# Kernel optimization log

Measured on AMD Instinct MI355X. Metric: run time of the kernel, lower is better.

Reference implementation:

```python
import jax, jax.numpy as jnp
import numpy as np

G = 4  # number of groups


def _group_vals(h, shift, Ua, Ua1, Ua2, Ua3):
    # h: [B, H]; Ua: [g, H/g, r]; Ua1/2/3: [g, r, H/g]
    B, H = h.shape
    hg = h.reshape(B, G, H // G)
    if shift:
        # torch index = rotate-left by `shift`: new group j reads old group (j+shift)%g
        hg = jnp.roll(hg, -shift, axis=1)
    t = jnp.einsum('bgd,gdr->bgr', hg, Ua)  # shared low-rank projection
    proj = lambda M: jnp.einsum('bgr,grd->bgd', t, M).reshape(B, H)
    return proj(Ua1), proj(Ua2), proj(Ua3)


def setup_inputs() -> dict:
    key = jax.random.key(0)
    ks = jax.random.split(key, 24)
    B, I, H, wR = 8192, 1024, 1024, 256
    hg = H // G
    r01, r23 = 64, 32
    d = {}
    d['x'] = jax.random.normal(ks[0], (B, I), dtype=jnp.float32)
    d['h'] = jax.random.normal(ks[1], (B, H), dtype=jnp.float32)
    d['W'] = 0.1 * jax.random.normal(ks[2], (I, wR), dtype=jnp.float32)
    d['W1'] = 0.1 * jax.random.normal(ks[3], (wR, H), dtype=jnp.float32)
    d['W2'] = 0.1 * jax.random.normal(ks[4], (wR, H), dtype=jnp.float32)
    d['W3'] = 0.1 * jax.random.normal(ks[5], (wR, H), dtype=jnp.float32)
    d['U'] = 0.1 * jax.random.normal(ks[6], (G, hg, r01), dtype=jnp.float32)
    d['U1'] = 0.1 * jax.random.normal(ks[7], (G, r01, hg), dtype=jnp.float32)
    d['U2'] = 0.1 * jax.random.normal(ks[8], (G, r01, hg), dtype=jnp.float32)
    d['U3'] = 0.1 * jax.random.normal(ks[9], (G, r01, hg), dtype=jnp.float32)
    d['UU'] = 0.1 * jax.random.normal(ks[10], (G, hg, r01), dtype=jnp.float32)
    d['UU1'] = 0.1 * jax.random.normal(ks[11], (G, r01, hg), dtype=jnp.float32)
    d['UU2'] = 0.1 * jax.random.normal(ks[12], (G, r01, hg), dtype=jnp.float32)
    d['UU3'] = 0.1 * jax.random.normal(ks[13], (G, r01, hg), dtype=jnp.float32)
    d['UUU'] = 0.1 * jax.random.normal(ks[14], (G, hg, r23), dtype=jnp.float32)
    d['UUU1'] = 0.1 * jax.random.normal(ks[15], (G, r23, hg), dtype=jnp.float32)
    d['UUU2'] = 0.1 * jax.random.normal(ks[16], (G, r23, hg), dtype=jnp.float32)
    d['UUU3'] = 0.1 * jax.random.normal(ks[17], (G, r23, hg), dtype=jnp.float32)
    d['UUUU'] = 0.1 * jax.random.normal(ks[18], (G, hg, r23), dtype=jnp.float32)
    d['UUUU1'] = 0.1 * jax.random.normal(ks[19], (G, r23, hg), dtype=jnp.float32)
    d['UUUU2'] = 0.1 * jax.random.normal(ks[20], (G, r23, hg), dtype=jnp.float32)
    d['UUUU3'] = 0.1 * jax.random.normal(ks[21], (G, r23, hg), dtype=jnp.float32)
    d['bias_r'] = jnp.ones((1, H), dtype=jnp.float32)
    d['bias_gate'] = jnp.ones((1, H), dtype=jnp.float32)
    d['bias_update'] = jnp.ones((1, H), dtype=jnp.float32)
    return d


def reference(x, h, W, W1, W2, W3, U, U1, U2, U3, UU, UU1, UU2, UU3,
              UUU, UUU1, UUU2, UUU3, UUUU, UUUU1, UUUU2, UUUU3,
              bias_r, bias_gate, bias_update):
    u1, u2, u3 = _group_vals(h, 0, U, U1, U2, U3)
    uu1, uu2, uu3 = _group_vals(h, 1, UU, UU1, UU2, UU3)
    uuu1, uuu2, uuu3 = _group_vals(h, 2, UUU, UUU1, UUU2, UUU3)
    uuuu1, uuuu2, uuuu3 = _group_vals(h, 3, UUUU, UUUU1, UUUU2, UUUU3)
    xw = x @ W  # [B, wRank]
    w1, w2, w3 = xw @ W1, xw @ W2, xw @ W3
    r = jax.nn.sigmoid(w1 + u1 + uu1 + uuu1 + uuuu1 + bias_r)
    z = jax.nn.sigmoid(w2 + u2 + uu2 + uuu2 + uuuu2 + bias_gate)
    c_tilda = jnp.tanh(w3 + r * (u3 + uu3 + uuu3 + uuuu3) + bias_update)
    return z * h + (1.0 - z) * c_tilda
```

## Files before the change

kernel.cpp:

```cpp
#include <hip/hip_runtime.h>

typedef short bf16x8 __attribute__((ext_vector_type(8)));
typedef float f32x4 __attribute__((ext_vector_type(4)));
typedef float f32x16 __attribute__((ext_vector_type(16)));

__device__ __forceinline__ unsigned short f2bf(float f) {
  union { float f; unsigned u; } c; c.f = f;
  unsigned u = c.u;
  u += 0x7FFFu + ((u >> 16) & 1u);
  return (unsigned short)(u >> 16);
}
__device__ __forceinline__ float bf2f(unsigned short h) {
  union { unsigned u; float f; } c; c.u = ((unsigned)h) << 16;
  return c.f;
}
__device__ __forceinline__ void split2(float v, unsigned short& hi, unsigned short& lo) {
  union { float f; unsigned u; } c; c.f = v;
  unsigned uh = c.u & 0xFFFF0000u;
  hi = (unsigned short)(uh >> 16);
  union { unsigned u; float f; } d; d.u = uh;
  lo = f2bf(v - d.f);
}
__device__ __forceinline__ void gload16(const void* g, void* l) {
  __builtin_amdgcn_global_load_lds((const __attribute__((address_space(1))) void*)g,
                                   (__attribute__((address_space(3))) void*)l, 16, 0, 0);
}
__device__ __forceinline__ float sigm(float x) { return 1.0f / (1.0f + __expf(-x)); }
__device__ __forceinline__ float tanha(float x) { return 1.0f - 2.0f / (1.0f + __expf(2.0f * x)); }

__device__ __forceinline__ size_t fragIdxA(int row, int col) {
  int mb = row >> 7, rb = (row >> 5) & 3, l5 = row & 31;
  int cc = col >> 6, k4 = (col >> 4) & 3, hi = (col >> 3) & 1, e = col & 7;
  return ((size_t)(mb * 20 + cc) * 16 + rb * 4 + k4) * 512 + (hi * 32 + l5) * 8 + e;
}

__global__ __launch_bounds__(256) void s123(
    const float* __restrict__ W,
    const float* __restrict__ U, const float* __restrict__ UU,
    const float* __restrict__ UUU, const float* __restrict__ UUUU,
    const float* __restrict__ W1, const float* __restrict__ W2, const float* __restrict__ W3,
    const float* __restrict__ A1, const float* __restrict__ A2, const float* __restrict__ A3,
    const float* __restrict__ B1, const float* __restrict__ B2, const float* __restrict__ B3,
    const float* __restrict__ C1, const float* __restrict__ C2, const float* __restrict__ C3,
    const float* __restrict__ D1, const float* __restrict__ D2, const float* __restrict__ D3,
    unsigned short* __restrict__ Wt, unsigned short* __restrict__ Bg,
    unsigned short* __restrict__ Btp) {
  int gidx = blockIdx.x * 256 + threadIdx.x;
  if (gidx < 262144) {
    int idx = gidx;
    int n = idx >> 10, k = idx & 1023;
    Wt[idx] = f2bf(W[k * 256 + n]);
  } else if (gidx < 458752) {
    int idx = gidx - 262144;
    int g = idx / 49152;
    int rem = idx - g * 49152;
    int n = rem >> 8, k = rem & 255;
    int jj = 0, rr = n;
#pragma unroll
    for (int s = 0; s < 3; ++s) {
      int w = (((g - jj) & 3) < 2) ? 64 : 32;
      if (rr >= w) { rr -= w; ++jj; }
    }
    int v = (g - jj) & 3;
    int rv = (v < 2) ? 64 : 32;
    const float* M = (v == 0) ? U : (v == 1) ? UU : (v == 2) ? UUU : UUUU;
    Bg[idx] = f2bf(M[(jj * 256 + k) * rv + rr]);
  } else {
    int idx = gidx - 458752;
    int blk = idx / 12288;
    int w   = idx - blk * 12288;
    int frag = w >> 9, fl = (w >> 3) & 63, e = w & 7;
    int cb = blk & 3, jk = blk >> 2;
    int kt = jk % 11, j = jk / 11;
    int q = frag >> 3, colblk = (frag >> 2) & 1, k4 = frag & 3;
    int c  = cb * 64 + colblk * 32 + (fl & 31);
    int k2 = k4 * 16 + (fl >> 5) * 8 + e;
    float val;
    if (kt < 8) {
      int kk = (kt * 64 + k2) & 255;
      const float* Wp = (q == 0) ? W1 : (q == 1) ? W2 : W3;
      val = Wp[kk * 1024 + j * 256 + c];
    } else {
      int kT = (kt - 8) * 64 + k2;
      int v, r, rv;
      if (kT < 64)       { v = 0; r = kT;       rv = 64; }
      else if (kT < 128) { v = 1; r = kT - 64;  rv = 64; }
      else if (kT < 160) { v = 2; r = kT - 128; rv = 32; }
      else               { v = 3; r = kT - 160; rv = 32; }
      const float* M;
      if (v == 0)      M = (q == 0) ? A1 : (q == 1) ? A2 : A3;
      else if (v == 1) M = (q == 0) ? B1 : (q == 1) ? B2 : B3;
      else if (v == 2) M = (q == 0) ? C1 : (q == 1) ? C2 : C3;
      else             M = (q == 0) ? D1 : (q == 1) ? D2 : D3;
      val = M[(j * rv + r) * 256 + c];
    }
    Btp[idx] = f2bf(val);
  }
}

__global__ __launch_bounds__(256) void g1_xw(const float* __restrict__ x,
                                             const unsigned short* __restrict__ Wt,
                                             unsigned short* __restrict__ Abuf) {
  __shared__ char lds[49152];
  const int tid = threadIdx.x, lane = tid & 63, wid = tid >> 6;
  const int mb = blockIdx.x, nb = blockIdx.y;
  const int wn = wid;
  f32x4 acc[2][2] = {};
  float4 xr[2];
  const int r0 = tid >> 4, f4c = tid & 15;
  const float* xbase = x + (size_t)(mb * 32) * 1024 + f4c * 4;

  auto loadX = [&](int kt) {
#pragma unroll
    for (int q = 0; q < 2; ++q)
      xr[q] = *(const float4*)(xbase + (size_t)(q * 16 + r0) * 1024 + kt * 64);
  };
  auto writeA = [&](int buf) {
#pragma unroll
    for (int q = 0; q < 2; ++q) {
      int row = q * 16 + r0;
      float4 v = xr[q];
      unsigned short h0, h1, h2, h3, l0, l1, l2, l3;
      split2(v.x, h0, l0); split2(v.y, h1, l1);
      split2(v.z, h2, l2); split2(v.w, h3, l3);
      int ba = row * 128 + ((f4c * 8) ^ ((row & 7) << 4));
      *(uint2*)(lds + buf * 4096 + ba) =
          make_uint2(((unsigned)h1 << 16) | h0, ((unsigned)h3 << 16) | h2);
      *(uint2*)(lds + 8192 + buf * 4096 + ba) =
          make_uint2(((unsigned)l1 << 16) | l0, ((unsigned)l3 << 16) | l2);
    }
  };
  auto stageB = [&](int kt, int buf) {
#pragma unroll
    for (int it = 0; it < 4; ++it) {
      int nloc = it * 32 + wid * 8 + (lane >> 3);
      const char* src = (const char*)Wt + (size_t)(nb * 128 + nloc) * 2048 + kt * 128
                        + (((lane & 7) * 16) ^ ((nloc & 7) << 4));
      gload16(src, lds + 16384 + buf * 16384 + (it * 32 + wid * 8) * 128);
    }
  };

  loadX(0); stageB(0, 0); writeA(0);
  __syncthreads();
#pragma unroll 2
  for (int kt = 0; kt < 16; ++kt) {
    int buf = kt & 1;
    if (kt < 15) {
      loadX(kt + 1); stageB(kt + 1, buf ^ 1);
      asm volatile("s_waitcnt vmcnt(6)" ::: "memory");
    } else {
      asm volatile("s_waitcnt vmcnt(0)" ::: "memory");
    }
    __builtin_amdgcn_s_barrier();
    __builtin_amdgcn_sched_barrier(0);
    const char* hA = lds + buf * 4096;
    const char* lA = lds + 8192 + buf * 4096;
    const char* bB = lds + 16384 + buf * 16384;
#pragma unroll
    for (int ks = 0; ks < 2; ++ks) {
      bf16x8 ah[2], al[2], b[2];
#pragma unroll
      for (int mf = 0; mf < 2; ++mf) {
        int mloc = mf * 16 + (lane & 15);
        int ka = (ks * 64 + (lane >> 4) * 16) ^ ((mloc & 7) << 4);
        ah[mf] = *(const bf16x8*)(hA + mloc * 128 + ka);
        al[mf] = *(const bf16x8*)(lA + mloc * 128 + ka);
      }
#pragma unroll
      for (int nf = 0; nf < 2; ++nf) {
        int nloc = wn * 32 + nf * 16 + (lane & 15);
        int kb = (ks * 64 + (lane >> 4) * 16) ^ ((nloc & 7) << 4);
        b[nf] = *(const bf16x8*)(bB + nloc * 128 + kb);
      }
#pragma unroll
      for (int mf = 0; mf < 2; ++mf)
#pragma unroll
        for (int nf = 0; nf < 2; ++nf) {
          acc[mf][nf] = __builtin_amdgcn_mfma_f32_16x16x32_bf16(ah[mf], b[nf], acc[mf][nf], 0, 0, 0);
          acc[mf][nf] = __builtin_amdgcn_mfma_f32_16x16x32_bf16(al[mf], b[nf], acc[mf][nf], 0, 0, 0);
        }
    }
    if (kt < 15) writeA(buf ^ 1);
    __builtin_amdgcn_sched_barrier(0);
    asm volatile("s_waitcnt lgkmcnt(0)" ::: "memory");
    __builtin_amdgcn_s_barrier();
  }
#pragma unroll
  for (int mf = 0; mf < 2; ++mf)
#pragma unroll
    for (int nf = 0; nf < 2; ++nf)
#pragma unroll
      for (int r = 0; r < 4; ++r) {
        int row = mb * 32 + mf * 16 + (lane >> 4) * 4 + r;
        int col = nb * 128 + wn * 32 + nf * 16 + (lane & 15);
        float val = acc[mf][nf][r];
        unsigned short hi, lo;
        split2(val, hi, lo);
        Abuf[fragIdxA(row, col)] = hi;
        Abuf[fragIdxA(row, col + 256)] = lo;
      }
}

__global__ __launch_bounds__(256) void g2_t(const float* __restrict__ h,
                                            const unsigned short* __restrict__ Bg,
                                            unsigned short* __restrict__ Abuf) {
  __shared__ char lds[65536];
  const int tid = threadIdx.x, lane = tid & 63, wid = tid >> 6;
  const int mb = blockIdx.x, g = blockIdx.y;
  const int wm = wid >> 1, wn = wid & 1;
  f32x4 acc[2][6] = {};
  float4 hr[4];
  const int r0 = tid >> 4, f4c = tid & 15;
  const float* hbase = h + (size_t)(mb * 64) * 1024 + g * 256 + f4c * 4;

  auto loadH = [&](int kt) {
#pragma unroll
    for (int q = 0; q < 4; ++q)
      hr[q] = *(const float4*)(hbase + (size_t)(q * 16 + r0) * 1024 + kt * 64);
  };
  auto writeA = [&](int buf) {
#pragma unroll
    for (int q = 0; q < 4; ++q) {
      int row = q * 16 + r0;
      float4 v = hr[q];
      int ba = row * 128 + ((f4c * 8) ^ ((row & 7) << 4));
      *(uint2*)(lds + buf * 8192 + ba) =
          make_uint2(((unsigned)f2bf(v.y) << 16) | f2bf(v.x),
                     ((unsigned)f2bf(v.w) << 16) | f2bf(v.z));
    }
  };
  auto stageB = [&](int kt, int buf) {
#pragma unroll
    for (int it = 0; it < 6; ++it) {
      int nloc = it * 32 + wid * 8 + (lane >> 3);
      const char* src = (const char*)Bg + (size_t)(g * 192 + nloc) * 512 + kt * 128
                        + (((lane & 7) * 16) ^ ((nloc & 7) << 4));
      gload16(src, lds + 16384 + buf * 24576 + (it * 32 + wid * 8) * 128);
    }
  };

  loadH(0); stageB(0, 0); writeA(0);
  __syncthreads();
#pragma unroll
  for (int kt = 0; kt < 4; ++kt) {
    int buf = kt & 1;
    if (kt < 3) { loadH(kt + 1); stageB(kt + 1, buf ^ 1); }
    const char* cA = lds + buf * 8192;
    const char* cB = lds + 16384 + buf * 24576;
#pragma unroll
    for (int ks = 0; ks < 2; ++ks) {
      bf16x8 a[2], b[6];
#pragma unroll
      for (int mf = 0; mf < 2; ++mf) {
        int mloc = wm * 32 + mf * 16 + (lane & 15);
        int ka = (ks * 64 + (lane >> 4) * 16) ^ ((mloc & 7) << 4);
        a[mf] = *(const bf16x8*)(cA + mloc * 128 + ka);
      }
#pragma unroll
      for (int nf = 0; nf < 6; ++nf) {
        int nloc = wn * 96 + nf * 16 + (lane & 15);
        int kb = (ks * 64 + (lane >> 4) * 16) ^ ((nloc & 7) << 4);
        b[nf] = *(const bf16x8*)(cB + nloc * 128 + kb);
      }
#pragma unroll
      for (int mf = 0; mf < 2; ++mf)
#pragma unroll
        for (int nf = 0; nf < 6; ++nf)
          acc[mf][nf] = __builtin_amdgcn_mfma_f32_16x16x32_bf16(a[mf], b[nf], acc[mf][nf], 0, 0, 0);
    }
    if (kt < 3) writeA(buf ^ 1);
    __syncthreads();
  }
#pragma unroll
  for (int mf = 0; mf < 2; ++mf)
#pragma unroll
    for (int nf = 0; nf < 6; ++nf) {
      int n = wn * 96 + nf * 16 + (lane & 15);
      int jj = 0, rr = n;
#pragma unroll
      for (int s = 0; s < 3; ++s) {
        int w = (((g - jj) & 3) < 2) ? 64 : 32;
        if (rr >= w) { rr -= w; ++jj; }
      }
      int v = (g - jj) & 3;
      int offv = (v < 2) ? (v << 6) : (64 + (v << 5));
      int col = 512 + jj * 192 + offv + rr;
#pragma unroll
      for (int r = 0; r < 4; ++r) {
        int row = mb * 64 + wm * 32 + mf * 16 + (lane >> 4) * 4 + r;
        Abuf[fragIdxA(row, col)] = f2bf(acc[mf][nf][r]);
      }
    }
}

__global__ __launch_bounds__(256) void g3_main(const unsigned short* __restrict__ Abuf,
                                               const unsigned short* __restrict__ Btp,
                                               const float* __restrict__ h,
                                               const float* __restrict__ bias_r,
                                               const float* __restrict__ bias_g,
                                               const float* __restrict__ bias_u,
                                               float* __restrict__ out) {
  __shared__ char lds[81920];
  const int tid = threadIdx.x, lane = tid & 63, wid = tid >> 6;
  const int mb = blockIdx.x, cb = blockIdx.y, j = blockIdx.z;
  const int wm = wid >> 1, wn = wid & 1;
  f32x16 acc[2][4] = {};

  const char* AbufB = (const char*)Abuf;
  const char* BtpB  = (const char*)Btp;

  auto stage = [&](int kt, int buf) {
    int cc = (kt < 8) ? kt : (8 + j * 3 + (kt - 8));
    const char* asrc = AbufB + (size_t)(mb * 20 + cc) * 16384 + tid * 16;
    const char* bsrc = BtpB + (size_t)(((j * 11 + kt) * 4 + cb)) * 24576 + tid * 16;
#pragma unroll
    for (int it = 0; it < 4; ++it)
      gload16(asrc + it * 4096, lds + buf * 16384 + it * 4096 + wid * 1024);
#pragma unroll
    for (int it = 0; it < 6; ++it)
      gload16(bsrc + it * 4096, lds + 32768 + buf * 24576 + it * 4096 + wid * 1024);
  };

  stage(0, 0);
#pragma unroll
  for (int kt = 0; kt < 11; ++kt) {
    const int buf = kt & 1;
    if (kt < 10) {
      stage(kt + 1, buf ^ 1);
      asm volatile("s_waitcnt vmcnt(10)" ::: "memory");
    } else {
      asm volatile("s_waitcnt vmcnt(0)" ::: "memory");
    }
    __builtin_amdgcn_s_barrier();
    __builtin_amdgcn_sched_barrier(0);
    __builtin_amdgcn_s_setprio(1);
    const char* aB = lds + buf * 16384 + wm * 8192 + lane * 16;
    const char* bB = lds + 32768 + buf * 24576 + wn * 4096 + lane * 16;
#pragma unroll
    for (int k4 = 0; k4 < 4; ++k4) {
      bf16x8 a0 = *(const bf16x8*)(aB + k4 * 1024);
      bf16x8 a1 = *(const bf16x8*)(aB + 4096 + k4 * 1024);
#pragma unroll
      for (int q = 0; q < 3; ++q) {
        const int p = (kt < 8) ? q : ((q == 2) ? 3 : q);
        bf16x8 b = *(const bf16x8*)(bB + q * 8192 + k4 * 1024);
        acc[0][p] = __builtin_amdgcn_mfma_f32_32x32x16_bf16(a0, b, acc[0][p], 0, 0, 0);
        acc[1][p] = __builtin_amdgcn_mfma_f32_32x32x16_bf16(a1, b, acc[1][p], 0, 0, 0);
      }
    }
    __builtin_amdgcn_s_setprio(0);
    __builtin_amdgcn_sched_barrier(0);
    __builtin_amdgcn_s_barrier();
  }
  int cg = j * 256 + cb * 64 + wn * 32 + (lane & 31);
  float br = bias_r[cg], bg = bias_g[cg], bu = bias_u[cg];
#pragma unroll
  for (int mblk = 0; mblk < 2; ++mblk)
#pragma unroll
    for (int r = 0; r < 16; ++r) {
      int row = mb * 128 + wm * 64 + mblk * 32 + (r & 3) + 8 * (r >> 2) + 4 * (lane >> 5);
      float p0 = acc[mblk][0][r], p1 = acc[mblk][1][r];
      float p2 = acc[mblk][2][r], p3 = acc[mblk][3][r];
      float rr = sigm(p0 + br);
      float zz = sigm(p1 + bg);
      float ct = tanha(p2 + rr * p3 + bu);
      float hv = h[(size_t)row * 1024 + cg];
      out[(size_t)row * 1024 + cg] = zz * hv + (1.0f - zz) * ct;
    }
}

extern "C" void kernel_launch(void* const* d_in, const int* in_sizes, int n_in,
                              void* d_out, int out_size, void* d_ws, size_t ws_size,
                              hipStream_t stream) {
  const float* x   = (const float*)d_in[0];
  const float* h   = (const float*)d_in[1];
  const float* W   = (const float*)d_in[2];
  const float* W1  = (const float*)d_in[3];
  const float* W2  = (const float*)d_in[4];
  const float* W3  = (const float*)d_in[5];
  const float* U   = (const float*)d_in[6];
  const float* U1  = (const float*)d_in[7];
  const float* U2  = (const float*)d_in[8];
  const float* U3  = (const float*)d_in[9];
  const float* UU   = (const float*)d_in[10];
  const float* UU1  = (const float*)d_in[11];
  const float* UU2  = (const float*)d_in[12];
  const float* UU3  = (const float*)d_in[13];
  const float* UUU   = (const float*)d_in[14];
  const float* UUU1  = (const float*)d_in[15];
  const float* UUU2  = (const float*)d_in[16];
  const float* UUU3  = (const float*)d_in[17];
  const float* UUUU   = (const float*)d_in[18];
  const float* UUUU1  = (const float*)d_in[19];
  const float* UUUU2  = (const float*)d_in[20];
  const float* UUUU3  = (const float*)d_in[21];
  const float* bias_r = (const float*)d_in[22];
  const float* bias_g = (const float*)d_in[23];
  const float* bias_u = (const float*)d_in[24];

  char* ws = (char*)d_ws;
  unsigned short* Abuf = (unsigned short*)(ws);
  unsigned short* Wt   = (unsigned short*)(ws + 20971520);
  unsigned short* Bg   = (unsigned short*)(ws + 21495808);
  unsigned short* Btp  = (unsigned short*)(ws + 21889024);
  float* out = (float*)d_out;

  s123<<<10240, 256, 0, stream>>>(W, U, UU, UUU, UUUU,
                                  W1, W2, W3, U1, U2, U3, UU1, UU2, UU3,
                                  UUU1, UUU2, UUU3, UUUU1, UUUU2, UUUU3,
                                  Wt, Bg, Btp);
  g1_xw<<<dim3(256, 2), 256, 0, stream>>>(x, Wt, Abuf);
  g2_t<<<dim3(128, 4), 256, 0, stream>>>(h, Bg, Abuf);
  g3_main<<<dim3(64, 4, 4), 256, 0, stream>>>(Abuf, Btp, h, bias_r, bias_g, bias_u, out);
}
```

Baseline: 94.70 us.

## Widen g1 tile to full N and remap g3 blocks per XCD

```diff
diff --git a/kernel.cpp b/kernel.cpp
--- a/kernel.cpp
+++ b/kernel.cpp
@@ -101,11 +101,11 @@
 __global__ __launch_bounds__(256) void g1_xw(const float* __restrict__ x,
                                              const unsigned short* __restrict__ Wt,
                                              unsigned short* __restrict__ Abuf) {
-  __shared__ char lds[49152];
+  __shared__ char lds[81920];
   const int tid = threadIdx.x, lane = tid & 63, wid = tid >> 6;
-  const int mb = blockIdx.x, nb = blockIdx.y;
-  const int wn = wid;
-  f32x4 acc[2][2] = {};
+  const int mb = blockIdx.x;
+  const int wm = wid >> 1, wn = wid & 1;
+  f32x4 acc[8] = {};
   float4 xr[2];
   const int r0 = tid >> 4, f4c = tid & 15;
   const float* xbase = x + (size_t)(mb * 32) * 1024 + f4c * 4;
@@ -132,22 +132,21 @@
   };
   auto stageB = [&](int kt, int buf) {
 #pragma unroll
-    for (int it = 0; it < 4; ++it) {
+    for (int it = 0; it < 8; ++it) {
       int nloc = it * 32 + wid * 8 + (lane >> 3);
-      const char* src = (const char*)Wt + (size_t)(nb * 128 + nloc) * 2048 + kt * 128
+      const char* src = (const char*)Wt + (size_t)nloc * 2048 + kt * 128
                         + (((lane & 7) * 16) ^ ((nloc & 7) << 4));
-      gload16(src, lds + 16384 + buf * 16384 + (it * 32 + wid * 8) * 128);
+      gload16(src, lds + 16384 + buf * 32768 + (it * 32 + wid * 8) * 128);
     }
   };
 
   loadX(0); stageB(0, 0); writeA(0);
   __syncthreads();
-#pragma unroll 2
   for (int kt = 0; kt < 16; ++kt) {
     int buf = kt & 1;
     if (kt < 15) {
       loadX(kt + 1); stageB(kt + 1, buf ^ 1);
-      asm volatile("s_waitcnt vmcnt(6)" ::: "memory");
+      asm volatile("s_waitcnt vmcnt(10)" ::: "memory");
     } else {
       asm volatile("s_waitcnt vmcnt(0)" ::: "memory");
     }
@@ -155,30 +154,21 @@
     __builtin_amdgcn_sched_barrier(0);
     const char* hA = lds + buf * 4096;
     const char* lA = lds + 8192 + buf * 4096;
-    const char* bB = lds + 16384 + buf * 16384;
+    const char* bB = lds + 16384 + buf * 32768;
 #pragma unroll
     for (int ks = 0; ks < 2; ++ks) {
-      bf16x8 ah[2], al[2], b[2];
-#pragma unroll
-      for (int mf = 0; mf < 2; ++mf) {
-        int mloc = mf * 16 + (lane & 15);
-        int ka = (ks * 64 + (lane >> 4) * 16) ^ ((mloc & 7) << 4);
-        ah[mf] = *(const bf16x8*)(hA + mloc * 128 + ka);
-        al[mf] = *(const bf16x8*)(lA + mloc * 128 + ka);
-      }
-#pragma unroll
-      for (int nf = 0; nf < 2; ++nf) {
-        int nloc = wn * 32 + nf * 16 + (lane & 15);
+      int mloc = wm * 16 + (lane & 15);
+      int ka = (ks * 64 + (lane >> 4) * 16) ^ ((mloc & 7) << 4);
+      bf16x8 ah = *(const bf16x8*)(hA + mloc * 128 + ka);
+      bf16x8 al = *(const bf16x8*)(lA + mloc * 128 + ka);
+#pragma unroll
+      for (int nf = 0; nf < 8; ++nf) {
+        int nloc = wn * 128 + nf * 16 + (lane & 15);
         int kb = (ks * 64 + (lane >> 4) * 16) ^ ((nloc & 7) << 4);
-        b[nf] = *(const bf16x8*)(bB + nloc * 128 + kb);
-      }
-#pragma unroll
-      for (int mf = 0; mf < 2; ++mf)
-#pragma unroll
-        for (int nf = 0; nf < 2; ++nf) {
-          acc[mf][nf] = __builtin_amdgcn_mfma_f32_16x16x32_bf16(ah[mf], b[nf], acc[mf][nf], 0, 0, 0);
-          acc[mf][nf] = __builtin_amdgcn_mfma_f32_16x16x32_bf16(al[mf], b[nf], acc[mf][nf], 0, 0, 0);
-        }
+        bf16x8 b = *(const bf16x8*)(bB + nloc * 128 + kb);
+        acc[nf] = __builtin_amdgcn_mfma_f32_16x16x32_bf16(ah, b, acc[nf], 0, 0, 0);
+        acc[nf] = __builtin_amdgcn_mfma_f32_16x16x32_bf16(al, b, acc[nf], 0, 0, 0);
+      }
     }
     if (kt < 15) writeA(buf ^ 1);
     __builtin_amdgcn_sched_barrier(0);
@@ -186,19 +176,17 @@
     __builtin_amdgcn_s_barrier();
   }
 #pragma unroll
-  for (int mf = 0; mf < 2; ++mf)
-#pragma unroll
-    for (int nf = 0; nf < 2; ++nf)
-#pragma unroll
-      for (int r = 0; r < 4; ++r) {
-        int row = mb * 32 + mf * 16 + (lane >> 4) * 4 + r;
-        int col = nb * 128 + wn * 32 + nf * 16 + (lane & 15);
-        float val = acc[mf][nf][r];
-        unsigned short hi, lo;
-        split2(val, hi, lo);
-        Abuf[fragIdxA(row, col)] = hi;
-        Abuf[fragIdxA(row, col + 256)] = lo;
-      }
+  for (int nf = 0; nf < 8; ++nf)
+#pragma unroll
+    for (int r = 0; r < 4; ++r) {
+      int row = mb * 32 + wm * 16 + (lane >> 4) * 4 + r;
+      int col = wn * 128 + nf * 16 + (lane & 15);
+      float val = acc[nf][r];
+      unsigned short hi, lo;
+      split2(val, hi, lo);
+      Abuf[fragIdxA(row, col)] = hi;
+      Abuf[fragIdxA(row, col + 256)] = lo;
+    }
 }
 
 __global__ __launch_bounds__(256) void g2_t(const float* __restrict__ h,
@@ -302,7 +290,11 @@
                                                float* __restrict__ out) {
   __shared__ char lds[81920];
   const int tid = threadIdx.x, lane = tid & 63, wid = tid >> 6;
-  const int mb = blockIdx.x, cb = blockIdx.y, j = blockIdx.z;
+  const int flat = blockIdx.x;
+  const int xcd = flat & 7, idx = flat >> 3;
+  const int mb = xcd * 8 + (idx & 7);
+  const int cj = idx >> 3;
+  const int cb = cj & 3, j = cj >> 2;
   const int wm = wid >> 1, wn = wid & 1;
   f32x16 acc[2][4] = {};
 
@@ -409,7 +401,7 @@
                                   W1, W2, W3, U1, U2, U3, UU1, UU2, UU3,
                                   UUU1, UUU2, UUU3, UUUU1, UUUU2, UUUU3,
                                   Wt, Bg, Btp);
-  g1_xw<<<dim3(256, 2), 256, 0, stream>>>(x, Wt, Abuf);
+  g1_xw<<<256, 256, 0, stream>>>(x, Wt, Abuf);
   g2_t<<<dim3(128, 4), 256, 0, stream>>>(h, Bg, Abuf);
-  g3_main<<<dim3(64, 4, 4), 256, 0, stream>>>(Abuf, Btp, h, bias_r, bias_g, bias_u, out);
-}
+  g3_main<<<1024, 256, 0, stream>>>(Abuf, Btp, h, bias_r, bias_g, bias_u, out);
+}
```

Result: slower. 99.63 us (+5.2%).

## Merge xW and h-projection kernels, remap g3 blocks per XCD, restructure prefetch

Applied to the files above, without the earlier changes.

```diff
diff --git a/kernel.cpp b/kernel.cpp
--- a/kernel.cpp
+++ b/kernel.cpp
@@ -98,17 +98,17 @@
   }
 }
 
-__global__ __launch_bounds__(256) void g1_xw(const float* __restrict__ x,
-                                             const unsigned short* __restrict__ Wt,
-                                             unsigned short* __restrict__ Abuf) {
-  __shared__ char lds[49152];
-  const int tid = threadIdx.x, lane = tid & 63, wid = tid >> 6;
-  const int mb = blockIdx.x, nb = blockIdx.y;
-  const int wn = wid;
+__device__ __forceinline__ void g1_body(const float* __restrict__ x,
+                                        const unsigned short* __restrict__ Wt,
+                                        unsigned short* __restrict__ Abuf,
+                                        char* lds, int mb, int nb, int tid) {
+  const int lane = tid & 63, wid = tid >> 6;
+  const int wm = 0, wn = wid;
   f32x4 acc[2][2] = {};
   float4 xr[2];
   const int r0 = tid >> 4, f4c = tid & 15;
   const float* xbase = x + (size_t)(mb * 32) * 1024 + f4c * 4;
+  (void)wm;
 
   auto loadX = [&](int kt) {
 #pragma unroll
@@ -201,12 +201,11 @@
       }
 }
 
-__global__ __launch_bounds__(256) void g2_t(const float* __restrict__ h,
-                                            const unsigned short* __restrict__ Bg,
-                                            unsigned short* __restrict__ Abuf) {
-  __shared__ char lds[65536];
-  const int tid = threadIdx.x, lane = tid & 63, wid = tid >> 6;
-  const int mb = blockIdx.x, g = blockIdx.y;
+__device__ __forceinline__ void g2_body(const float* __restrict__ h,
+                                        const unsigned short* __restrict__ Bg,
+                                        unsigned short* __restrict__ Abuf,
+                                        char* lds, int mb, int g, int tid) {
+  const int lane = tid & 63, wid = tid >> 6;
   const int wm = wid >> 1, wn = wid & 1;
   f32x4 acc[2][6] = {};
   float4 hr[4];
@@ -291,6 +290,21 @@
         Abuf[fragIdxA(row, col)] = f2bf(acc[mf][nf][r]);
       }
     }
+}
+
+__global__ __launch_bounds__(256) void g12(const float* __restrict__ x,
+                                           const unsigned short* __restrict__ Wt,
+                                           const float* __restrict__ h,
+                                           const unsigned short* __restrict__ Bg,
+                                           unsigned short* __restrict__ Abuf) {
+  __shared__ char lds[65536];
+  int b = blockIdx.x, tid = threadIdx.x;
+  if (b < 512) {
+    g1_body(x, Wt, Abuf, lds, b >> 1, b & 1, tid);
+  } else {
+    int b2 = b - 512;
+    g2_body(h, Bg, Abuf, lds, b2 >> 2, b2 & 3, tid);
+  }
 }
 
 __global__ __launch_bounds__(256) void g3_main(const unsigned short* __restrict__ Abuf,
@@ -302,7 +316,11 @@
                                                float* __restrict__ out) {
   __shared__ char lds[81920];
   const int tid = threadIdx.x, lane = tid & 63, wid = tid >> 6;
-  const int mb = blockIdx.x, cb = blockIdx.y, j = blockIdx.z;
+  const int flat = blockIdx.x;
+  const int xcd = flat & 7, idx = flat >> 3;
+  const int mb = xcd * 8 + (idx & 7);
+  const int cj = idx >> 3;
+  const int cb = cj & 3, j = cj >> 2;
   const int wm = wid >> 1, wn = wid & 1;
   f32x16 acc[2][4] = {};
 
@@ -325,14 +343,10 @@
 #pragma unroll
   for (int kt = 0; kt < 11; ++kt) {
     const int buf = kt & 1;
-    if (kt < 10) {
-      stage(kt + 1, buf ^ 1);
-      asm volatile("s_waitcnt vmcnt(10)" ::: "memory");
-    } else {
-      asm volatile("s_waitcnt vmcnt(0)" ::: "memory");
-    }
+    asm volatile("s_waitcnt vmcnt(0)" ::: "memory");
     __builtin_amdgcn_s_barrier();
     __builtin_amdgcn_sched_barrier(0);
+    if (kt < 10) stage(kt + 1, buf ^ 1);
     __builtin_amdgcn_s_setprio(1);
     const char* aB = lds + buf * 16384 + wm * 8192 + lane * 16;
     const char* bB = lds + 32768 + buf * 24576 + wn * 4096 + lane * 16;
@@ -350,7 +364,6 @@
     }
     __builtin_amdgcn_s_setprio(0);
     __builtin_amdgcn_sched_barrier(0);
-    __builtin_amdgcn_s_barrier();
   }
   int cg = j * 256 + cb * 64 + wn * 32 + (lane & 31);
   float br = bias_r[cg], bg = bias_g[cg], bu = bias_u[cg];
@@ -409,7 +422,6 @@
                                   W1, W2, W3, U1, U2, U3, UU1, UU2, UU3,
                                   UUU1, UUU2, UUU3, UUUU1, UUUU2, UUUU3,
                                   Wt, Bg, Btp);
-  g1_xw<<<dim3(256, 2), 256, 0, stream>>>(x, Wt, Abuf);
-  g2_t<<<dim3(128, 4), 256, 0, stream>>>(h, Bg, Abuf);
-  g3_main<<<dim3(64, 4, 4), 256, 0, stream>>>(Abuf, Btp, h, bias_r, bias_g, bias_u, out);
-}
+  g12<<<1024, 256, 0, stream>>>(x, Wt, h, Bg, Abuf);
+  g3_main<<<1024, 256, 0, stream>>>(Abuf, Btp, h, bias_r, bias_g, bias_u, out);
+}
```

After: 93.99 us. Within noise of the previous version (-0.7%).
